# Optimization experiments

Measured on AMD Instinct MI355X. Metric: run time of the kernel, lower is better.

The kernel has to match this reference:

```python
import jax, jax.numpy as jnp
import numpy as np

EPS = 1e-07


def setup_inputs() -> dict:
    dim, degree, Bv = 512, 8, 16384
    key = jax.random.key(0)
    kx, kc = jax.random.split(key)
    x = jax.random.normal(kx, (Bv, dim), dtype=jnp.float32)
    # init std matches nn.init.normal_(std=1/(dim*(degree+1)))
    cheby_coeffs = jax.random.normal(kc, (dim, dim, degree + 1), dtype=jnp.float32) / (dim * (degree + 1))
    return {"x": x, "cheby_coeffs": cheby_coeffs}


def reference(x, cheby_coeffs):
    # x: (Bv, dim); cheby_coeffs: (dim, dim, K) with K = degree+1
    K = cheby_coeffs.shape[-1]
    ar = jnp.arange(K, dtype=x.dtype)  # (K,)
    t = jnp.clip(jnp.tanh(x), -1.0 + EPS, 1.0 - EPS)  # (Bv, dim)
    theta = jnp.arccos(t)  # (Bv, dim)
    cheb = jnp.cos(theta[:, :, None] * ar)  # (Bv, dim, K) Chebyshev basis T_k(tanh x)
    y = jnp.einsum('bik,ijk->bj', cheb, cheby_coeffs)
    return y
```

## Files before the change

### kernel.cpp

```cpp
#include <hip/hip_runtime.h>
#include <hip/hip_bf16.h>


typedef __bf16 bf16x8 __attribute__((ext_vector_type(8)));
typedef __bf16 bf16x4 __attribute__((ext_vector_type(4)));
typedef float  f32x4  __attribute__((ext_vector_type(4)));

#define DIM  512
#define KDEG 9
#define NK   8
#define NIC  16
#define SLAB (4 * DIM * 8)

__global__ void pack_w_kernel(const float* __restrict__ coeffs,
                              __bf16* __restrict__ W2) {
    int t  = blockIdx.x * blockDim.x + threadIdx.x;
    int j  = t & (DIM - 1);
    int s  = (t >> 9) & 3;
    int ic = t >> 11;

    bf16x8 v[KDEG];
#pragma unroll
    for (int e = 0; e < 8; ++e) {
        int i = ic * 32 + s * 8 + e;
        const float* src = coeffs + ((size_t)i * DIM + j) * KDEG;
#pragma unroll
        for (int k = 0; k < KDEG; ++k)
            v[k][e] = (__bf16)src[k];
    }
#pragma unroll
    for (int k = 0; k < KDEG; ++k) {
        size_t off = (size_t)(k * 16 + ic) * SLAB + ((size_t)s * DIM + j) * 8;
        *reinterpret_cast<bf16x8*>(W2 + off) = v[k];
    }
}

__global__ void s0_kernel(const float* __restrict__ coeffs,
                          float* __restrict__ S0) {
    const int j    = blockIdx.x;
    const int lane = threadIdx.x;
    float s = 0.0f;
#pragma unroll
    for (int i = lane; i < DIM; i += 64)
        s += coeffs[((size_t)i * DIM + j) * KDEG];
#pragma unroll
    for (int off = 32; off > 0; off >>= 1)
        s += __shfl_down(s, off, 64);
    if (lane == 0) S0[j] = s;
}

__global__ __launch_bounds__(512, 4) void cheby_gemm_kernel(
    const float* __restrict__ x,
    const __bf16* __restrict__ W2,
    float* __restrict__ out)
{
    __shared__ __bf16 A_lds[2][NK][64][4][8];

    const int tid   = threadIdx.x;
    const int lane  = tid & 63;
    const int wid   = tid >> 6;
    const int l15   = lane & 15;
    const int l4    = lane >> 4;
    const int nhalf = blockIdx.x & 1;
    const int bm    = (blockIdx.x >> 1) * 64;
    const int cb    = nhalf * 256 + wid * 32;

    const int prow  = tid >> 3;
    const int pi4   = (tid & 7) * 4;
    const int pslot = pi4 >> 3;
    const int phalf = (pi4 >> 2) & 1;
    const int rsw   = (prow >> 1) & 3;
    __bf16* wp = &A_lds[0][0][prow][pslot ^ rsw][phalf * 4];
    const float* xp = x + (size_t)(bm + prow) * DIM + pi4;

    const __bf16* abase = &A_lds[0][0][l15][l4 ^ ((l15 >> 1) & 3)][0];

    const __bf16* wbase = W2 + ((size_t)l4 * DIM + cb + l15) * 8;

    const float* S0 = (const float*)W2;
    f32x4 acc[4][2];
#pragma unroll
    for (int nf = 0; nf < 2; ++nf) {
        float s0v = S0[cb + nf * 16 + l15];
#pragma unroll
        for (int mf = 0; mf < 4; ++mf)
#pragma unroll
            for (int r = 0; r < 4; ++r)
                acc[mf][nf][r] = s0v;
    }

    f32x4 xq = *reinterpret_cast<const f32x4*>(xp);
    {
        float Tk[4], Tm[4], t2[4];
#pragma unroll
        for (int e = 0; e < 4; ++e) {
            float p = __builtin_amdgcn_exp2f(xq[e] * 2.8853900817779268f);
            float t = 1.0f - 2.0f * __builtin_amdgcn_rcpf(p + 1.0f);
            Tk[e] = t;  t2[e] = t + t;  Tm[e] = 1.0f;
        }
#pragma unroll
        for (int kk = 0; kk < NK; ++kk) {
            bf16x4 v;
#pragma unroll
            for (int e = 0; e < 4; ++e) v[e] = (__bf16)Tk[e];
            *reinterpret_cast<bf16x4*>(wp + kk * 2048) = v;
            if (kk < NK - 1) {
#pragma unroll
                for (int e = 0; e < 4; ++e) {
                    float Tn = __builtin_fmaf(t2[e], Tk[e], -Tm[e]);
                    Tm[e] = Tk[e];  Tk[e] = Tn;
                }
            }
        }
    }
    xq = *reinterpret_cast<const f32x4*>(xp + 32);

    bf16x8 bq[4][2];
#pragma unroll
    for (int s = 0; s < 3; ++s)
#pragma unroll
        for (int nf = 0; nf < 2; ++nf)
            bq[s][nf] = *reinterpret_cast<const bf16x8*>(
                wbase + (size_t)((s + 1) * 16) * SLAB + nf * 128);

    asm volatile("s_waitcnt lgkmcnt(0)" ::: "memory");
    __builtin_amdgcn_s_barrier();

    float Tk[4], Tm[4], t2[4];

#define BODY(BUF, IC, PROD, XLOAD, PREFX)                                        \
    {                                                                            \
        _Pragma("unroll")                                                        \
        for (int k = 1; k <= NK; ++k) {                                          \
                               \
            if (k <= 5 || PREFX) {                                               \
                const int nk  = (k <= 5) ? k + 3 : k - 5;                        \
                const int nic = (k <= 5) ? (IC) : (IC) + 1;                      \
                const __bf16* np = wbase + (size_t)(nk * 16 + nic) * SLAB;       \
                _Pragma("unroll")                                                \
                for (int nf = 0; nf < 2; ++nf)                                   \
                    bq[(k + 2) & 3][nf] =                                        \
                        *reinterpret_cast<const bf16x8*>(np + nf * 128);         \
            }                                                                    \
                                  \
            bf16x8 af[4];                                                        \
            _Pragma("unroll")                                                    \
            for (int mf = 0; mf < 4; ++mf)                                       \
                af[mf] = *reinterpret_cast<const bf16x8*>(                       \
                    abase + (BUF) * 16384 + (k - 1) * 2048 + mf * 512);          \
                                                      \
            _Pragma("unroll")                                                    \
            for (int nf = 0; nf < 2; ++nf)                                       \
                _Pragma("unroll")                                                \
                for (int mf = 0; mf < 4; ++mf)                                   \
                    acc[mf][nf] = __builtin_amdgcn_mfma_f32_16x16x32_bf16(       \
                        af[mf], bq[(k - 1) & 3][nf], acc[mf][nf], 0, 0, 0);      \
                          \
            if (PROD) {                                                          \
                if (k == 1) {                                                    \
                    _Pragma("unroll")                                            \
                    for (int e = 0; e < 4; ++e) {                                \
                        float p = __builtin_amdgcn_exp2f(                        \
                            xq[e] * 2.8853900817779268f);                        \
                        float t = 1.0f - 2.0f * __builtin_amdgcn_rcpf(p + 1.0f); \
                        Tk[e] = t;  t2[e] = t + t;  Tm[e] = 1.0f;                \
                    }                                                            \
                } else {                                                         \
                    _Pragma("unroll")                                            \
                    for (int e = 0; e < 4; ++e) {                                \
                        float Tn = __builtin_fmaf(t2[e], Tk[e], -Tm[e]);         \
                        Tm[e] = Tk[e];  Tk[e] = Tn;                              \
                    }                                                            \
                }                                                                \
                bf16x4 v;                                                        \
                _Pragma("unroll")                                                \
                for (int e = 0; e < 4; ++e) v[e] = (__bf16)Tk[e];                \
                *reinterpret_cast<bf16x4*>(                                      \
                    wp + (1 - (BUF)) * 16384 + (k - 1) * 2048) = v;              \
            }                                                                    \
            if (XLOAD && k == 2)                                                 \
                xq = *reinterpret_cast<const f32x4*>(xp + ((IC) + 2) * 32);      \
        }                                                                        \
        if (PROD) {                                                              \
            asm volatile("s_waitcnt lgkmcnt(0)" ::: "memory");                   \
            __builtin_amdgcn_s_barrier();                                        \
        }                                                                        \
    }

    for (int icp = 0; icp < 14; icp += 2) {
        BODY(0, icp,     1, 1, 1);
        BODY(1, icp + 1, 1, 1, 1);
    }
    BODY(0, 14, 1, 0, 1);
    BODY(1, 15, 0, 0, 0);
#undef BODY

#pragma unroll
    for (int mf = 0; mf < 4; ++mf)
#pragma unroll
        for (int r = 0; r < 4; ++r) {
            const int row = bm + mf * 16 + l4 * 4 + r;
            float* orow = out + (size_t)row * DIM + cb + l15;
#pragma unroll
            for (int nf = 0; nf < 2; ++nf)
                orow[nf * 16] = acc[mf][nf][r];
        }
}

extern "C" void kernel_launch(void* const* d_in, const int* in_sizes, int n_in,
                              void* d_out, int out_size, void* d_ws, size_t ws_size,
                              hipStream_t stream) {
    const float* x      = (const float*)d_in[0];
    const float* coeffs = (const float*)d_in[1];
    float* out          = (float*)d_out;
    __bf16* W2          = (__bf16*)d_ws;

    pack_w_kernel<<<(DIM * 64) / 256, 256, 0, stream>>>(coeffs, W2);
    s0_kernel<<<DIM, 64, 0, stream>>>(coeffs, (float*)W2);

    cheby_gemm_kernel<<<512, 512, 0, stream>>>(x, W2, out);
}
```

Before: 80.12 us.

## Halve block to 4 waves with 64-column wave tiles and MFMA priority boost

Each block now uses 256 threads (4 waves) instead of 8, and each wave computes a 64x64 output tile (4x4 MFMA fragments) instead of 64x32. Each thread now produces 8 Chebyshev values per row chunk and writes them with bf16x8 LDS stores. This doubles register reuse of the A fragments per B load and halves the redundant basis generation per block. s_setprio is raised around the MFMA burst to favor matrix issue. The cost is higher register pressure, lower occupancy, and fewer waves available to hide latency.

```diff
diff --git a/kernel.cpp b/kernel.cpp
--- a/kernel.cpp
+++ b/kernel.cpp
@@ -3,7 +3,6 @@
 
 
 typedef __bf16 bf16x8 __attribute__((ext_vector_type(8)));
-typedef __bf16 bf16x4 __attribute__((ext_vector_type(4)));
 typedef float  f32x4  __attribute__((ext_vector_type(4)));
 
 #define DIM  512
@@ -49,7 +48,7 @@
     if (lane == 0) S0[j] = s;
 }
 
-__global__ __launch_bounds__(512, 4) void cheby_gemm_kernel(
+__global__ __launch_bounds__(256, 2) void cheby_gemm_kernel(
     const float* __restrict__ x,
     const __bf16* __restrict__ W2,
     float* __restrict__ out)
@@ -63,24 +62,22 @@
     const int l4    = lane >> 4;
     const int nhalf = blockIdx.x & 1;
     const int bm    = (blockIdx.x >> 1) * 64;
-    const int cb    = nhalf * 256 + wid * 32;
-
-    const int prow  = tid >> 3;
-    const int pi4   = (tid & 7) * 4;
-    const int pslot = pi4 >> 3;
-    const int phalf = (pi4 >> 2) & 1;
-    const int rsw   = (prow >> 1) & 3;
-    __bf16* wp = &A_lds[0][0][prow][pslot ^ rsw][phalf * 4];
-    const float* xp = x + (size_t)(bm + prow) * DIM + pi4;
+    const int cb    = nhalf * 256 + wid * 64;
+
+    const int prow = tid >> 2;
+    const int ps   = tid & 3;
+    const int rsw  = (prow >> 1) & 3;
+    __bf16* wp = &A_lds[0][0][prow][ps ^ rsw][0];
+    const float* xp = x + (size_t)(bm + prow) * DIM + ps * 8;
 
     const __bf16* abase = &A_lds[0][0][l15][l4 ^ ((l15 >> 1) & 3)][0];
 
     const __bf16* wbase = W2 + ((size_t)l4 * DIM + cb + l15) * 8;
 
     const float* S0 = (const float*)W2;
-    f32x4 acc[4][2];
-#pragma unroll
-    for (int nf = 0; nf < 2; ++nf) {
+    f32x4 acc[4][4];
+#pragma unroll
+    for (int nf = 0; nf < 4; ++nf) {
         float s0v = S0[cb + nf * 16 + l15];
 #pragma unroll
         for (int mf = 0; mf < 4; ++mf)
@@ -89,44 +86,47 @@
                 acc[mf][nf][r] = s0v;
     }
 
-    f32x4 xq = *reinterpret_cast<const f32x4*>(xp);
+    f32x4 xqa = *reinterpret_cast<const f32x4*>(xp);
+    f32x4 xqb = *reinterpret_cast<const f32x4*>(xp + 4);
     {
-        float Tk[4], Tm[4], t2[4];
-#pragma unroll
-        for (int e = 0; e < 4; ++e) {
-            float p = __builtin_amdgcn_exp2f(xq[e] * 2.8853900817779268f);
+        float Tk[8], Tm[8], t2[8];
+#pragma unroll
+        for (int e = 0; e < 8; ++e) {
+            float xv = (e < 4) ? xqa[e] : xqb[e - 4];
+            float p = __builtin_amdgcn_exp2f(xv * 2.8853900817779268f);
             float t = 1.0f - 2.0f * __builtin_amdgcn_rcpf(p + 1.0f);
             Tk[e] = t;  t2[e] = t + t;  Tm[e] = 1.0f;
         }
 #pragma unroll
         for (int kk = 0; kk < NK; ++kk) {
-            bf16x4 v;
-#pragma unroll
-            for (int e = 0; e < 4; ++e) v[e] = (__bf16)Tk[e];
-            *reinterpret_cast<bf16x4*>(wp + kk * 2048) = v;
+            bf16x8 v;
+#pragma unroll
+            for (int e = 0; e < 8; ++e) v[e] = (__bf16)Tk[e];
+            *reinterpret_cast<bf16x8*>(wp + kk * 2048) = v;
             if (kk < NK - 1) {
 #pragma unroll
-                for (int e = 0; e < 4; ++e) {
+                for (int e = 0; e < 8; ++e) {
                     float Tn = __builtin_fmaf(t2[e], Tk[e], -Tm[e]);
                     Tm[e] = Tk[e];  Tk[e] = Tn;
                 }
             }
         }
     }
-    xq = *reinterpret_cast<const f32x4*>(xp + 32);
-
-    bf16x8 bq[4][2];
+    xqa = *reinterpret_cast<const f32x4*>(xp + 32);
+    xqb = *reinterpret_cast<const f32x4*>(xp + 36);
+
+    bf16x8 bq[4][4];
 #pragma unroll
     for (int s = 0; s < 3; ++s)
 #pragma unroll
-        for (int nf = 0; nf < 2; ++nf)
+        for (int nf = 0; nf < 4; ++nf)
             bq[s][nf] = *reinterpret_cast<const bf16x8*>(
                 wbase + (size_t)((s + 1) * 16) * SLAB + nf * 128);
 
     asm volatile("s_waitcnt lgkmcnt(0)" ::: "memory");
     __builtin_amdgcn_s_barrier();
 
-    float Tk[4], Tm[4], t2[4];
+    float Tk[8], Tm[8], t2[8];
 
 #define BODY(BUF, IC, PROD, XLOAD, PREFX)                                        \
     {                                                                            \
@@ -138,7 +138,7 @@
                 const int nic = (k <= 5) ? (IC) : (IC) + 1;                      \
                 const __bf16* np = wbase + (size_t)(nk * 16 + nic) * SLAB;       \
                 _Pragma("unroll")                                                \
-                for (int nf = 0; nf < 2; ++nf)                                   \
+                for (int nf = 0; nf < 4; ++nf)                                   \
                     bq[(k + 2) & 3][nf] =                                        \
                         *reinterpret_cast<const bf16x8*>(np + nf * 128);         \
             }                                                                    \
@@ -148,38 +148,43 @@
             for (int mf = 0; mf < 4; ++mf)                                       \
                 af[mf] = *reinterpret_cast<const bf16x8*>(                       \
                     abase + (BUF) * 16384 + (k - 1) * 2048 + mf * 512);          \
-                                                      \
+                                                     \
+            __builtin_amdgcn_s_setprio(1);                                       \
             _Pragma("unroll")                                                    \
-            for (int nf = 0; nf < 2; ++nf)                                       \
+            for (int nf = 0; nf < 4; ++nf)                                       \
                 _Pragma("unroll")                                                \
                 for (int mf = 0; mf < 4; ++mf)                                   \
                     acc[mf][nf] = __builtin_amdgcn_mfma_f32_16x16x32_bf16(       \
                         af[mf], bq[(k - 1) & 3][nf], acc[mf][nf], 0, 0, 0);      \
+            __builtin_amdgcn_s_setprio(0);                                       \
                           \
             if (PROD) {                                                          \
                 if (k == 1) {                                                    \
                     _Pragma("unroll")                                            \
-                    for (int e = 0; e < 4; ++e) {                                \
+                    for (int e = 0; e < 8; ++e) {                                \
+                        float xv = (e < 4) ? xqa[e] : xqb[e - 4];                \
                         float p = __builtin_amdgcn_exp2f(                        \
-                            xq[e] * 2.8853900817779268f);                        \
+                            xv * 2.8853900817779268f);                           \
                         float t = 1.0f - 2.0f * __builtin_amdgcn_rcpf(p + 1.0f); \
                         Tk[e] = t;  t2[e] = t + t;  Tm[e] = 1.0f;                \
                     }                                                            \
                 } else {                                                         \
                     _Pragma("unroll")                                            \
-                    for (int e = 0; e < 4; ++e) {                                \
+                    for (int e = 0; e < 8; ++e) {                                \
                         float Tn = __builtin_fmaf(t2[e], Tk[e], -Tm[e]);         \
                         Tm[e] = Tk[e];  Tk[e] = Tn;                              \
                     }                                                            \
                 }                                                                \
-                bf16x4 v;                                                        \
+                bf16x8 v;                                                        \
                 _Pragma("unroll")                                                \
-                for (int e = 0; e < 4; ++e) v[e] = (__bf16)Tk[e];                \
-                *reinterpret_cast<bf16x4*>(                                      \
+                for (int e = 0; e < 8; ++e) v[e] = (__bf16)Tk[e];                \
+                *reinterpret_cast<bf16x8*>(                                      \
                     wp + (1 - (BUF)) * 16384 + (k - 1) * 2048) = v;              \
             }                                                                    \
-            if (XLOAD && k == 2)                                                 \
-                xq = *reinterpret_cast<const f32x4*>(xp + ((IC) + 2) * 32);      \
+            if (XLOAD && k == 2) {                                               \
+                xqa = *reinterpret_cast<const f32x4*>(xp + ((IC) + 2) * 32);     \
+                xqb = *reinterpret_cast<const f32x4*>(xp + ((IC) + 2) * 32 + 4); \
+            }                                                                    \
         }                                                                        \
         if (PROD) {                                                              \
             asm volatile("s_waitcnt lgkmcnt(0)" ::: "memory");                   \
@@ -202,7 +207,7 @@
             const int row = bm + mf * 16 + l4 * 4 + r;
             float* orow = out + (size_t)row * DIM + cb + l15;
 #pragma unroll
-            for (int nf = 0; nf < 2; ++nf)
+            for (int nf = 0; nf < 4; ++nf)
                 orow[nf * 16] = acc[mf][nf][r];
         }
 }
@@ -218,5 +223,5 @@
     pack_w_kernel<<<(DIM * 64) / 256, 256, 0, stream>>>(coeffs, W2);
     s0_kernel<<<DIM, 64, 0, stream>>>(coeffs, (float*)W2);
 
-    cheby_gemm_kernel<<<512, 512, 0, stream>>>(x, W2, out);
-}
+    cheby_gemm_kernel<<<512, 256, 0, stream>>>(x, W2, out);
+}
```

Result: faster. 77.11 us (-3.8%).
